# Kernel optimization log

Hardware: AMD Instinct MI355X
Metric: run time of the kernel (lower is better)

Reference implementation:

```python
import jax, jax.numpy as jnp
import numpy as np

NUM_FEATURES = 1_000_000  # np.max(999999)+1
EMBED_DIM = 64
NUM_FIELDS = 39
BATCH = 16384


def setup_inputs() -> dict:
    key = jax.random.key(0)
    k_x, k_e, k_b, k_w = jax.random.split(key, 4)
    x = jax.random.randint(k_x, (BATCH, NUM_FIELDS), 0, NUM_FEATURES, dtype=jnp.int64 if jax.config.jax_enable_x64 else jnp.int32)
    # trunc_normal_(std=0.01) ~ small normal init; plain normal*0.01 is fine for a numeric reference
    embeddings = jax.random.normal(k_e, (NUM_FEATURES, EMBED_DIM), dtype=jnp.float32) * 0.01
    bias = jax.random.normal(k_b, (NUM_FEATURES, 1), dtype=jnp.float32) * 0.01
    field_inter_weights = jax.random.normal(k_w, (NUM_FIELDS, NUM_FIELDS), dtype=jnp.float32) * 0.01
    w0 = jnp.zeros((1,), dtype=jnp.float32)
    return {"x": x, "embeddings": embeddings, "bias": bias,
            "field_inter_weights": field_inter_weights, "w0": w0}


def reference(x, embeddings, bias, field_inter_weights, w0):
    # emb: (B, F, D) gathered rows
    emb = embeddings[x]
    # bias lookup -> (B, F), summed over fields
    biases_sum = bias[x][..., 0].sum(axis=1)  # (B,)
    # zero the diagonal of the field interaction weight matrix
    W = field_inter_weights - jnp.diag(jnp.diag(field_inter_weights))  # (F, F)
    # batched Gram matrix emb @ emb^T : (B, F, F)
    gram = jnp.einsum('bid,bjd->bij', emb, emb)
    inter = 0.5 * jnp.einsum('bij,ij->b', gram, W)  # weighted sum over both field dims
    return w0 + biases_sum + inter  # (B,)
```

## Files before the change

### kernel.cpp

```cpp
#include <hip/hip_runtime.h>


constexpr int NF   = 39;
constexpr int D    = 64;
constexpr int IPAD = 48;
constexpr int EST  = D + 4;
constexpr int NT   = 256;

__global__ __launch_bounds__(NT) void fwfm_kernel(
    const int*   __restrict__ x,
    const float* __restrict__ emb,
    const float* __restrict__ bias,
    const float* __restrict__ W,
    const float* __restrict__ w0,
    float*       __restrict__ out)
{
    __shared__ float sE[IPAD * EST];
    __shared__ float sW[IPAD * NF];
    __shared__ int   sIdx[NF];
    __shared__ float sRed[NT / 64];

    const int b = blockIdx.x;
    const int t = threadIdx.x;

    if (t < NF) sIdx[t] = x[(size_t)b * NF + t];

    for (int u = t; u < IPAD * NF; u += NT) {
        int i = u / NF;
        int j = u - i * NF;
        sW[u] = (i < NF && i != j) ? W[i * NF + j] : 0.0f;
    }
    for (int u = t; u < (IPAD - NF) * 16; u += NT) {
        int r = NF + (u >> 4), c = u & 15;
        *(float4*)(sE + r * EST + c * 4) = make_float4(0.f, 0.f, 0.f, 0.f);
    }
    __syncthreads();

    for (int u = t; u < NF * 16; u += NT) {
        int r = u >> 4, c = u & 15;
        const float4* src = (const float4*)(emb + (size_t)sIdx[r] * D);
        *(float4*)(sE + r * EST + c * 4) = src[c];
    }
    float bsum = (t < NF) ? bias[(size_t)sIdx[t]] : 0.0f;
    __syncthreads();

    const int g  = t >> 4;
    const int h  = t & 15;
    const int i0 = g * 3;
    const float4 e0 = *(const float4*)(sE + (i0 + 0) * EST + h * 4);
    const float4 e1 = *(const float4*)(sE + (i0 + 1) * EST + h * 4);
    const float4 e2 = *(const float4*)(sE + (i0 + 2) * EST + h * 4);

    float acc = 0.0f;
    #pragma unroll 3
    for (int j = 0; j < NF; ++j) {
        const float4 ej = *(const float4*)(sE + j * EST + h * 4);
        const float w0v = sW[(i0 + 0) * NF + j];
        const float w1v = sW[(i0 + 1) * NF + j];
        const float w2v = sW[(i0 + 2) * NF + j];
        float d0 = ej.x * e0.x + ej.y * e0.y + ej.z * e0.z + ej.w * e0.w;
        float d1 = ej.x * e1.x + ej.y * e1.y + ej.z * e1.z + ej.w * e1.w;
        float d2 = ej.x * e2.x + ej.y * e2.y + ej.z * e2.z + ej.w * e2.w;
        acc = fmaf(w0v, d0, acc);
        acc = fmaf(w1v, d1, acc);
        acc = fmaf(w2v, d2, acc);
    }
    acc = 0.5f * acc + bsum;

    #pragma unroll
    for (int off = 32; off > 0; off >>= 1)
        acc += __shfl_down(acc, off, 64);
    if ((t & 63) == 0) sRed[t >> 6] = acc;
    __syncthreads();
    if (t == 0) {
        float tot = 0.0f;
        #pragma unroll
        for (int wv = 0; wv < NT / 64; ++wv) tot += sRed[wv];
        out[b] = w0[0] + tot;
    }
}

extern "C" void kernel_launch(void* const* d_in, const int* in_sizes, int n_in,
                              void* d_out, int out_size, void* d_ws, size_t ws_size,
                              hipStream_t stream) {
    const int*   x    = (const int*)d_in[0];
    const float* emb  = (const float*)d_in[1];
    const float* bias = (const float*)d_in[2];
    const float* W    = (const float*)d_in[3];
    const float* w0   = (const float*)d_in[4];
    float*       out  = (float*)d_out;

    const int batch = out_size;
    fwfm_kernel<<<batch, NT, 0, stream>>>(x, emb, bias, W, w0, out);
}
```

Baseline: 387.9 us.

## Compute FwFM per wave with register-resident embeddings and quadratic-form reduction

Replaces the one-block-per-sample shared-memory Gram computation with one wave per sample. Each lane holds one embedding dimension for all 39 fields in registers and computes the quadratic form e^T W e directly, so there is no shared memory and no block barriers. A small prep kernel writes the diagonal-zeroed, transposed, padded W into workspace so it can be read as uniform scalar loads. Every lane now does about 1.5k FMAs, and the 39-element register arrays add register pressure. Each lane also re-reads x and bias redundantly, though these loads should be broadcast.

```diff
diff --git a/kernel.cpp b/kernel.cpp
--- a/kernel.cpp
+++ b/kernel.cpp
@@ -1,83 +1,74 @@
 #include <hip/hip_runtime.h>
 
 
-constexpr int NF   = 39;
-constexpr int D    = 64;
-constexpr int IPAD = 48;
-constexpr int EST  = D + 4;
-constexpr int NT   = 256;
+constexpr int NF = 39;
+constexpr int D  = 64;
+constexpr int WP = 40;
+constexpr int WAVES_PER_BLOCK = 4;
+constexpr int NT = 64 * WAVES_PER_BLOCK;
+
+__global__ __launch_bounds__(256) void prep_w(const float* __restrict__ W,
+                                              float* __restrict__ Wp) {
+    int t = blockIdx.x * blockDim.x + threadIdx.x;
+    if (t < WP * WP) {
+        int j = t / WP, i = t - j * WP;
+        float v = 0.0f;
+        if (i < NF && j < NF && i != j) v = W[j * NF + i];
+        Wp[t] = v;
+    }
+}
 
 __global__ __launch_bounds__(NT) void fwfm_kernel(
     const int*   __restrict__ x,
     const float* __restrict__ emb,
     const float* __restrict__ bias,
-    const float* __restrict__ W,
+    const float* __restrict__ Wp,
     const float* __restrict__ w0,
     float*       __restrict__ out)
 {
-    __shared__ float sE[IPAD * EST];
-    __shared__ float sW[IPAD * NF];
-    __shared__ int   sIdx[NF];
-    __shared__ float sRed[NT / 64];
+    const int lane = threadIdx.x & 63;
+    const int wave = __builtin_amdgcn_readfirstlane((int)(threadIdx.x >> 6));
+    const int b    = blockIdx.x * WAVES_PER_BLOCK + wave;
 
-    const int b = blockIdx.x;
-    const int t = threadIdx.x;
+    const int* xrow = x + (size_t)b * NF;
 
-    if (t < NF) sIdx[t] = x[(size_t)b * NF + t];
+    int idx[NF];
+    #pragma unroll
+    for (int f = 0; f < NF; ++f) idx[f] = xrow[f];
 
-    for (int u = t; u < IPAD * NF; u += NT) {
-        int i = u / NF;
-        int j = u - i * NF;
-        sW[u] = (i < NF && i != j) ? W[i * NF + j] : 0.0f;
+    float E[NF];
+    #pragma unroll
+    for (int f = 0; f < NF; ++f)
+        E[f] = emb[(size_t)idx[f] * D + lane];
+
+    float bsum = 0.0f;
+    #pragma unroll
+    for (int f = 0; f < NF; ++f) bsum += bias[idx[f]];
+
+    float q = 0.0f;
+    #pragma unroll
+    for (int j = 0; j < NF; ++j) {
+        const float* wr = Wp + j * WP;
+        float s0 = 0.0f, s1 = 0.0f, s2 = 0.0f, s3 = 0.0f;
+        #pragma unroll
+        for (int i = 0; i < 36; i += 4) {
+            s0 = fmaf(wr[i + 0], E[i + 0], s0);
+            s1 = fmaf(wr[i + 1], E[i + 1], s1);
+            s2 = fmaf(wr[i + 2], E[i + 2], s2);
+            s3 = fmaf(wr[i + 3], E[i + 3], s3);
+        }
+        s0 = fmaf(wr[36], E[36], s0);
+        s1 = fmaf(wr[37], E[37], s1);
+        s2 = fmaf(wr[38], E[38], s2);
+        q  = fmaf(E[j], (s0 + s1) + (s2 + s3), q);
     }
-    for (int u = t; u < (IPAD - NF) * 16; u += NT) {
-        int r = NF + (u >> 4), c = u & 15;
-        *(float4*)(sE + r * EST + c * 4) = make_float4(0.f, 0.f, 0.f, 0.f);
-    }
-    __syncthreads();
-
-    for (int u = t; u < NF * 16; u += NT) {
-        int r = u >> 4, c = u & 15;
-        const float4* src = (const float4*)(emb + (size_t)sIdx[r] * D);
-        *(float4*)(sE + r * EST + c * 4) = src[c];
-    }
-    float bsum = (t < NF) ? bias[(size_t)sIdx[t]] : 0.0f;
-    __syncthreads();
-
-    const int g  = t >> 4;
-    const int h  = t & 15;
-    const int i0 = g * 3;
-    const float4 e0 = *(const float4*)(sE + (i0 + 0) * EST + h * 4);
-    const float4 e1 = *(const float4*)(sE + (i0 + 1) * EST + h * 4);
-    const float4 e2 = *(const float4*)(sE + (i0 + 2) * EST + h * 4);
-
-    float acc = 0.0f;
-    #pragma unroll 3
-    for (int j = 0; j < NF; ++j) {
-        const float4 ej = *(const float4*)(sE + j * EST + h * 4);
-        const float w0v = sW[(i0 + 0) * NF + j];
-        const float w1v = sW[(i0 + 1) * NF + j];
-        const float w2v = sW[(i0 + 2) * NF + j];
-        float d0 = ej.x * e0.x + ej.y * e0.y + ej.z * e0.z + ej.w * e0.w;
-        float d1 = ej.x * e1.x + ej.y * e1.y + ej.z * e1.z + ej.w * e1.w;
-        float d2 = ej.x * e2.x + ej.y * e2.y + ej.z * e2.z + ej.w * e2.w;
-        acc = fmaf(w0v, d0, acc);
-        acc = fmaf(w1v, d1, acc);
-        acc = fmaf(w2v, d2, acc);
-    }
-    acc = 0.5f * acc + bsum;
 
     #pragma unroll
     for (int off = 32; off > 0; off >>= 1)
-        acc += __shfl_down(acc, off, 64);
-    if ((t & 63) == 0) sRed[t >> 6] = acc;
-    __syncthreads();
-    if (t == 0) {
-        float tot = 0.0f;
-        #pragma unroll
-        for (int wv = 0; wv < NT / 64; ++wv) tot += sRed[wv];
-        out[b] = w0[0] + tot;
-    }
+        q += __shfl_down(q, off, 64);
+
+    if (lane == 0)
+        out[b] = w0[0] + bsum + 0.5f * q;
 }
 
 extern "C" void kernel_launch(void* const* d_in, const int* in_sizes, int n_in,
@@ -89,7 +80,10 @@
     const float* W    = (const float*)d_in[3];
     const float* w0   = (const float*)d_in[4];
     float*       out  = (float*)d_out;
+    float*       Wp   = (float*)d_ws;
+
+    prep_w<<<(WP * WP + 255) / 256, 256, 0, stream>>>(W, Wp);
 
     const int batch = out_size;
-    fwfm_kernel<<<batch, NT, 0, stream>>>(x, emb, bias, W, w0, out);
+    fwfm_kernel<<<batch / WAVES_PER_BLOCK, NT, 0, stream>>>(x, emb, bias, Wp, w0, out);
 }
```

Result: no change. 386.1 us (-0.5%).
